# Performance work log

Measured on AMD Instinct MI355X. Metric: run time of the kernel, lower is better.

## Reference

```python
import jax, jax.numpy as jnp
import numpy as np
import math

B, H, S, D = 2, 16, 2048, 64

def setup_inputs() -> dict:
    key = jax.random.key(0)
    kq, kk, kv = jax.random.split(key, 3)
    Q = jax.random.normal(kq, (B, H, S, D), dtype=jnp.float32)
    K = jax.random.normal(kk, (B, H, S, D), dtype=jnp.float32)
    V = jax.random.normal(kv, (B, H, S, D), dtype=jnp.float32)
    # causal mask, broadcastable over batch and heads; 0 -> masked out
    mask = jnp.tril(jnp.ones((S, S), dtype=jnp.int32))[None, None, :, :]
    return {"Q": Q, "K": K, "V": V, "mask": mask}

def reference(Q, K, V, mask):
    d_k = Q.shape[-1]
    # scores: [B, H, S, S]
    scores = jnp.einsum("bhqd,bhkd->bhqk", Q, K) / math.sqrt(d_k)
    scores = jnp.where(mask == 0, jnp.float32(-1e9), scores)
    attn_weights = jax.nn.softmax(scores, axis=-1)
    output = jnp.einsum("bhqk,bhkd->bhqd", attn_weights, V)
    return (output, attn_weights)
```

## Files before the change

kernel.cpp:

```cpp
#include <hip/hip_runtime.h>
#include <hip/hip_bf16.h>


#define S_ 2048
#define D_ 64
#define BH_ 32

typedef short short8 __attribute__((ext_vector_type(8)));
typedef float f32x4 __attribute__((ext_vector_type(4)));
typedef unsigned short ushort4v __attribute__((ext_vector_type(4)));

__device__ __forceinline__ unsigned short f2bf(float f) {
  union { float f; unsigned u; } c; c.f = f;
  unsigned u = c.u + 0x7fffu + ((c.u >> 16) & 1u);
  return (unsigned short)(u >> 16);
}

__device__ __forceinline__ void g2l16(const void* g, void* l) {
  __builtin_amdgcn_global_load_lds(
      (const __attribute__((address_space(1))) unsigned int*)g,
      (__attribute__((address_space(3))) unsigned int*)l, 16, 0, 0);
}

__global__ __launch_bounds__(256) void cvt_bf16(const float* __restrict__ src,
                                                unsigned short* __restrict__ dst, int n4) {
  int i = blockIdx.x * 256 + threadIdx.x;
  if (i < n4) {
    float4 v = ((const float4*)src)[i];
    ushort4v u = { f2bf(v.x), f2bf(v.y), f2bf(v.z), f2bf(v.w) };
    ((ushort4v*)dst)[i] = u;
  }
}

__global__ __launch_bounds__(256) void vtrans(const float* __restrict__ V,
                                              unsigned short* __restrict__ Vt) {
  __shared__ float T[64][65];
  const int bh = blockIdx.x >> 5, st = blockIdx.x & 31;
  const int tid = threadIdx.x;
  const float* src = V + ((size_t)bh * S_ + st * 64) * D_;
  for (int i = tid; i < 1024; i += 256) {
    int e = i * 4; int r = e >> 6; int c = e & 63;
    float4 v = *(const float4*)(src + e);
    T[r][c] = v.x; T[r][c + 1] = v.y; T[r][c + 2] = v.z; T[r][c + 3] = v.w;
  }
  __syncthreads();
  const int d = tid >> 2;
  const int sc = (tid & 3) * 16;
  unsigned short* dst = Vt + ((size_t)bh * D_ + d) * S_ + st * 64 + sc;
#pragma unroll
  for (int j = 0; j < 16; ++j) dst[j] = f2bf(T[sc + j][d]);
}

__global__ __launch_bounds__(256, 4)
void sdpa_main(const unsigned short* __restrict__ Qg, const unsigned short* __restrict__ Kg,
               const unsigned short* __restrict__ Vtg, float* __restrict__ Og,
               float* __restrict__ Pg) {
  __shared__ __align__(16) unsigned short Kb2[2][64 * 64];
  __shared__ __align__(16) unsigned short Vb2[2][64 * 64];
  __shared__ __align__(16) unsigned short Ps[64 * 64];

  const int tid = threadIdx.x;
  const int wave = tid >> 6;
  const int lane = tid & 63;
  const int m = lane & 15;
  const int quad = lane >> 4;

  const int bh = blockIdx.x & 31;
  const int t = blockIdx.x >> 5;
  const int sg = t >> 3, g = t & 7;
  const int qb = (sg == 0) ? 16 + g : (sg == 1) ? 31 - g : (sg == 2) ? 15 - g : g;
  const int q0 = qb * 64;
  const int ktiles = qb + 1;

  const unsigned short* Kbh = Kg + (size_t)bh * S_ * D_;
  const unsigned short* Vbh = Vtg + (size_t)bh * D_ * S_;

  const unsigned short* Qrow = Qg + ((size_t)bh * S_ + q0 + wave * 16 + m) * D_;
  const short8 qf0 = *(const short8*)(Qrow + quad * 8);
  const short8 qf1 = *(const short8*)(Qrow + 32 + quad * 8);

  auto stageK = [&](const unsigned short* gbase, unsigned short* lbase) {
#pragma unroll
    for (int j = 0; j < 2; ++j) {
      int gi = wave * 2 + j;
      int row = gi * 8 + (lane >> 3);
      int c = (lane & 7) ^ (row & 7);
      g2l16(gbase + row * 64 + c * 8, lbase + gi * 512);
    }
  };
  auto stageV = [&](int kt, unsigned short* lbase) {
#pragma unroll
    for (int j = 0; j < 2; ++j) {
      int gi = wave * 2 + j;
      int d = gi * 8 + (lane >> 3);
      int c = (lane & 7) ^ (d & 7);
      g2l16(Vbh + (size_t)d * S_ + kt * 64 + c * 8, lbase + gi * 512);
    }
  };
  auto frag = [&](const unsigned short* base, int row, int kc) -> short8 {
    int c = (kc * 4 + quad) ^ (row & 7);
    return *(const short8*)(base + row * 64 + c * 8);
  };

  stageK(Kbh, Kb2[0]);
  {
    const int zc4 = (31 - qb) * 16;
    if (zc4 > 0) {
      f32x4 z = {0.f, 0.f, 0.f, 0.f};
      float* base = Pg + ((size_t)(bh * S_ + q0 + wave * 16)) * S_ + (q0 + 64);
#pragma unroll 1
      for (int r = 0; r < 16; ++r)
        for (int i = lane; i < zc4; i += 64)
          __builtin_nontemporal_store(z, (f32x4*)(base + (size_t)r * S_ + i * 4));
    }
  }

  float lsum[4] = {0.f, 0.f, 0.f, 0.f};
  for (int kt = 0; kt < ktiles; ++kt) {
    __syncthreads();
    if (kt + 1 < ktiles) stageK(Kbh + (kt + 1) * 64 * 64, Kb2[(kt + 1) & 1]);
    const unsigned short* Kt = Kb2[kt & 1];
    const bool diag = (kt == qb);
#pragma unroll
    for (int nt = 0; nt < 4; ++nt) {
      f32x4 acc = {0.f, 0.f, 0.f, 0.f};
      acc = __builtin_amdgcn_mfma_f32_16x16x32_bf16(qf0, frag(Kt, nt * 16 + m, 0), acc, 0, 0, 0);
      acc = __builtin_amdgcn_mfma_f32_16x16x32_bf16(qf1, frag(Kt, nt * 16 + m, 1), acc, 0, 0, 0);
      if (diag) {
        const int kg = kt * 64 + nt * 16 + m;
#pragma unroll
        for (int r = 0; r < 4; ++r) {
          const int qg = q0 + wave * 16 + quad * 4 + r;
          lsum[r] += (kg > qg) ? 0.f : __expf(acc[r] * 0.125f);
        }
      } else {
#pragma unroll
        for (int r = 0; r < 4; ++r) lsum[r] += __expf(acc[r] * 0.125f);
      }
    }
  }

  __syncthreads();
  stageK(Kbh, Kb2[0]);
  stageV(0, Vb2[0]);

  float invl[4];
#pragma unroll
  for (int r = 0; r < 4; ++r) {
    float v = lsum[r];
    v += __shfl_xor(v, 1); v += __shfl_xor(v, 2);
    v += __shfl_xor(v, 4); v += __shfl_xor(v, 8);
    invl[r] = 1.0f / v;
  }

  f32x4 oacc[4];
#pragma unroll
  for (int dt = 0; dt < 4; ++dt) oacc[dt] = (f32x4){0.f, 0.f, 0.f, 0.f};

  for (int kt = 0; kt < ktiles; ++kt) {
    __syncthreads();
    if (kt + 1 < ktiles) {
      stageK(Kbh + (kt + 1) * 64 * 64, Kb2[(kt + 1) & 1]);
      stageV(kt + 1, Vb2[(kt + 1) & 1]);
    }
    const unsigned short* Kt = Kb2[kt & 1];
    const unsigned short* Vt = Vb2[kt & 1];
    const bool diag = (kt == qb);
#pragma unroll
    for (int nt = 0; nt < 4; ++nt) {
      f32x4 acc = {0.f, 0.f, 0.f, 0.f};
      acc = __builtin_amdgcn_mfma_f32_16x16x32_bf16(qf0, frag(Kt, nt * 16 + m, 0), acc, 0, 0, 0);
      acc = __builtin_amdgcn_mfma_f32_16x16x32_bf16(qf1, frag(Kt, nt * 16 + m, 1), acc, 0, 0, 0);
      const int kg = kt * 64 + nt * 16 + m;
#pragma unroll
      for (int r = 0; r < 4; ++r) {
        const int qg = q0 + wave * 16 + quad * 4 + r;
        float p = (diag && kg > qg) ? 0.f : __expf(acc[r] * 0.125f) * invl[r];
        __builtin_nontemporal_store(p, Pg + (size_t)(bh * S_ + qg) * S_ + kg);
        const int prow = wave * 16 + quad * 4 + r;
        const int pcol = nt * 16 + m;
        Ps[prow * 64 + (pcol & 7) + ((((pcol >> 3) ^ (prow & 7))) << 3)] = f2bf(p);
      }
    }
#pragma unroll
    for (int dt = 0; dt < 4; ++dt)
#pragma unroll
      for (int kc = 0; kc < 2; ++kc) {
        const int prow = wave * 16 + m;
        short8 a = *(const short8*)&Ps[prow * 64 + (((kc * 4 + quad) ^ (prow & 7)) << 3)];
        short8 b = frag(Vt, dt * 16 + m, kc);
        oacc[dt] = __builtin_amdgcn_mfma_f32_16x16x32_bf16(a, b, oacc[dt], 0, 0, 0);
      }
  }

#pragma unroll
  for (int dt = 0; dt < 4; ++dt)
#pragma unroll
    for (int r = 0; r < 4; ++r)
      Og[(size_t)(bh * S_ + q0 + wave * 16 + quad * 4 + r) * D_ + dt * 16 + m] =
          oacc[dt][r];
}

extern "C" void kernel_launch(void* const* d_in, const int* in_sizes, int n_in,
                              void* d_out, int out_size, void* d_ws, size_t ws_size,
                              hipStream_t stream) {
  const float* Q = (const float*)d_in[0];
  const float* K = (const float*)d_in[1];
  const float* V = (const float*)d_in[2];
  float* Og = (float*)d_out;
  float* Pg = (float*)d_out + (size_t)BH_ * S_ * D_;

  unsigned short* Qbf = (unsigned short*)d_ws;
  unsigned short* Kbf = Qbf + (size_t)BH_ * S_ * D_;
  unsigned short* Vt  = Kbf + (size_t)BH_ * S_ * D_;

  const int n4 = (BH_ * S_ * D_) / 4;
  cvt_bf16<<<dim3(n4 / 256), dim3(256), 0, stream>>>(Q, Qbf, n4);
  cvt_bf16<<<dim3(n4 / 256), dim3(256), 0, stream>>>(K, Kbf, n4);
  vtrans<<<dim3(1024), dim3(256), 0, stream>>>(V, Vt);
  sdpa_main<<<dim3(1024), dim3(256), 0, stream>>>(Qbf, Kbf, Vt, Og, Pg);
}
```

Baseline: 666.5 us.

## Drop the separate softmax-sum pass and normalize P in a follow-up kernel

The main kernel no longer runs a first pass over all K tiles just to accumulate the exp row sums. It now writes unnormalized exp scores to P and into the LDS P tile, accumulates the row sums during the single PV pass, and scales O by the inverse sum at the end. It also stores the inverse sums so a new pnorm kernel can reread and rescale the causal part of P. Q is converted to bf16 inside the main kernel, which removes its separate conversion launch. The cost is an extra read and write of roughly half of the P matrix, traded against half of the QK MFMA and exp work.

```diff
diff --git a/kernel.cpp b/kernel.cpp
--- a/kernel.cpp
+++ b/kernel.cpp
@@ -22,11 +22,16 @@
       (__attribute__((address_space(3))) unsigned int*)l, 16, 0, 0);
 }
 
+__device__ __forceinline__ int qb_of(int t) {
+  const int sg = t >> 3, g = t & 7;
+  return (sg == 0) ? 16 + g : (sg == 1) ? 31 - g : (sg == 2) ? 15 - g : g;
+}
+
 __global__ __launch_bounds__(256) void cvt_bf16(const float* __restrict__ src,
                                                 unsigned short* __restrict__ dst, int n4) {
   int i = blockIdx.x * 256 + threadIdx.x;
   if (i < n4) {
-    float4 v = ((const float4*)src)[i];
+    f32x4 v = ((const f32x4*)src)[i];
     ushort4v u = { f2bf(v.x), f2bf(v.y), f2bf(v.z), f2bf(v.w) };
     ((ushort4v*)dst)[i] = u;
   }
@@ -40,7 +45,7 @@
   const float* src = V + ((size_t)bh * S_ + st * 64) * D_;
   for (int i = tid; i < 1024; i += 256) {
     int e = i * 4; int r = e >> 6; int c = e & 63;
-    float4 v = *(const float4*)(src + e);
+    f32x4 v = *(const f32x4*)(src + e);
     T[r][c] = v.x; T[r][c + 1] = v.y; T[r][c + 2] = v.z; T[r][c + 3] = v.w;
   }
   __syncthreads();
@@ -52,9 +57,9 @@
 }
 
 __global__ __launch_bounds__(256, 4)
-void sdpa_main(const unsigned short* __restrict__ Qg, const unsigned short* __restrict__ Kg,
+void sdpa_main(const float* __restrict__ Qg, const unsigned short* __restrict__ Kg,
                const unsigned short* __restrict__ Vtg, float* __restrict__ Og,
-               float* __restrict__ Pg) {
+               float* __restrict__ Pg, float* __restrict__ Lg) {
   __shared__ __align__(16) unsigned short Kb2[2][64 * 64];
   __shared__ __align__(16) unsigned short Vb2[2][64 * 64];
   __shared__ __align__(16) unsigned short Ps[64 * 64];
@@ -66,18 +71,25 @@
   const int quad = lane >> 4;
 
   const int bh = blockIdx.x & 31;
-  const int t = blockIdx.x >> 5;
-  const int sg = t >> 3, g = t & 7;
-  const int qb = (sg == 0) ? 16 + g : (sg == 1) ? 31 - g : (sg == 2) ? 15 - g : g;
+  const int qb = qb_of(blockIdx.x >> 5);
   const int q0 = qb * 64;
   const int ktiles = qb + 1;
 
   const unsigned short* Kbh = Kg + (size_t)bh * S_ * D_;
   const unsigned short* Vbh = Vtg + (size_t)bh * D_ * S_;
 
-  const unsigned short* Qrow = Qg + ((size_t)bh * S_ + q0 + wave * 16 + m) * D_;
-  const short8 qf0 = *(const short8*)(Qrow + quad * 8);
-  const short8 qf1 = *(const short8*)(Qrow + 32 + quad * 8);
+  const float* Qrow = Qg + ((size_t)bh * S_ + q0 + wave * 16 + m) * D_;
+  short8 qf0, qf1;
+  {
+    f32x4 a0 = *(const f32x4*)(Qrow + quad * 8);
+    f32x4 a1 = *(const f32x4*)(Qrow + quad * 8 + 4);
+    f32x4 b0 = *(const f32x4*)(Qrow + 32 + quad * 8);
+    f32x4 b1 = *(const f32x4*)(Qrow + 32 + quad * 8 + 4);
+    qf0 = (short8){(short)f2bf(a0.x), (short)f2bf(a0.y), (short)f2bf(a0.z), (short)f2bf(a0.w),
+                   (short)f2bf(a1.x), (short)f2bf(a1.y), (short)f2bf(a1.z), (short)f2bf(a1.w)};
+    qf1 = (short8){(short)f2bf(b0.x), (short)f2bf(b0.y), (short)f2bf(b0.z), (short)f2bf(b0.w),
+                   (short)f2bf(b1.x), (short)f2bf(b1.y), (short)f2bf(b1.z), (short)f2bf(b1.w)};
+  }
 
   auto stageK = [&](const unsigned short* gbase, unsigned short* lbase) {
 #pragma unroll
@@ -103,6 +115,7 @@
   };
 
   stageK(Kbh, Kb2[0]);
+  stageV(0, Vb2[0]);
   {
     const int zc4 = (31 - qb) * 16;
     if (zc4 > 0) {
@@ -116,43 +129,6 @@
   }
 
   float lsum[4] = {0.f, 0.f, 0.f, 0.f};
-  for (int kt = 0; kt < ktiles; ++kt) {
-    __syncthreads();
-    if (kt + 1 < ktiles) stageK(Kbh + (kt + 1) * 64 * 64, Kb2[(kt + 1) & 1]);
-    const unsigned short* Kt = Kb2[kt & 1];
-    const bool diag = (kt == qb);
-#pragma unroll
-    for (int nt = 0; nt < 4; ++nt) {
-      f32x4 acc = {0.f, 0.f, 0.f, 0.f};
-      acc = __builtin_amdgcn_mfma_f32_16x16x32_bf16(qf0, frag(Kt, nt * 16 + m, 0), acc, 0, 0, 0);
-      acc = __builtin_amdgcn_mfma_f32_16x16x32_bf16(qf1, frag(Kt, nt * 16 + m, 1), acc, 0, 0, 0);
-      if (diag) {
-        const int kg = kt * 64 + nt * 16 + m;
-#pragma unroll
-        for (int r = 0; r < 4; ++r) {
-          const int qg = q0 + wave * 16 + quad * 4 + r;
-          lsum[r] += (kg > qg) ? 0.f : __expf(acc[r] * 0.125f);
-        }
-      } else {
-#pragma unroll
-        for (int r = 0; r < 4; ++r) lsum[r] += __expf(acc[r] * 0.125f);
-      }
-    }
-  }
-
-  __syncthreads();
-  stageK(Kbh, Kb2[0]);
-  stageV(0, Vb2[0]);
-
-  float invl[4];
-#pragma unroll
-  for (int r = 0; r < 4; ++r) {
-    float v = lsum[r];
-    v += __shfl_xor(v, 1); v += __shfl_xor(v, 2);
-    v += __shfl_xor(v, 4); v += __shfl_xor(v, 8);
-    invl[r] = 1.0f / v;
-  }
-
   f32x4 oacc[4];
 #pragma unroll
   for (int dt = 0; dt < 4; ++dt) oacc[dt] = (f32x4){0.f, 0.f, 0.f, 0.f};
@@ -175,11 +151,12 @@
 #pragma unroll
       for (int r = 0; r < 4; ++r) {
         const int qg = q0 + wave * 16 + quad * 4 + r;
-        float p = (diag && kg > qg) ? 0.f : __expf(acc[r] * 0.125f) * invl[r];
-        __builtin_nontemporal_store(p, Pg + (size_t)(bh * S_ + qg) * S_ + kg);
+        float e = (diag && kg > qg) ? 0.f : __expf(acc[r] * 0.125f);
+        lsum[r] += e;
+        __builtin_nontemporal_store(e, Pg + (size_t)(bh * S_ + qg) * S_ + kg);
         const int prow = wave * 16 + quad * 4 + r;
         const int pcol = nt * 16 + m;
-        Ps[prow * 64 + (pcol & 7) + ((((pcol >> 3) ^ (prow & 7))) << 3)] = f2bf(p);
+        Ps[prow * 64 + (pcol & 7) + ((((pcol >> 3) ^ (prow & 7))) << 3)] = f2bf(e);
       }
     }
 #pragma unroll
@@ -193,12 +170,45 @@
       }
   }
 
+  float invl[4];
+#pragma unroll
+  for (int r = 0; r < 4; ++r) {
+    float v = lsum[r];
+    v += __shfl_xor(v, 1); v += __shfl_xor(v, 2);
+    v += __shfl_xor(v, 4); v += __shfl_xor(v, 8);
+    invl[r] = 1.0f / v;
+  }
+  if (m == 0) {
+#pragma unroll
+    for (int r = 0; r < 4; ++r)
+      Lg[bh * S_ + q0 + wave * 16 + quad * 4 + r] = invl[r];
+  }
+
 #pragma unroll
   for (int dt = 0; dt < 4; ++dt)
 #pragma unroll
     for (int r = 0; r < 4; ++r)
       Og[(size_t)(bh * S_ + q0 + wave * 16 + quad * 4 + r) * D_ + dt * 16 + m] =
-          oacc[dt][r];
+          oacc[dt][r] * invl[r];
+}
+
+__global__ __launch_bounds__(256) void pnorm(float* __restrict__ Pg,
+                                             const float* __restrict__ Lg) {
+  const int bh = blockIdx.x & 31;
+  const int qb = qb_of(blockIdx.x >> 5);
+  const int len4 = (qb + 1) * 16;
+  float* base = Pg + ((size_t)(bh * S_ + qb * 64)) * S_;
+  const float* L = Lg + bh * S_ + qb * 64;
+#pragma unroll 1
+  for (int r = 0; r < 64; ++r) {
+    const float inv = L[r];
+    f32x4* rowp = (f32x4*)(base + (size_t)r * S_);
+    for (int i = threadIdx.x; i < len4; i += 256) {
+      f32x4 v = __builtin_nontemporal_load(rowp + i);
+      v.x *= inv; v.y *= inv; v.z *= inv; v.w *= inv;
+      __builtin_nontemporal_store(v, rowp + i);
+    }
+  }
 }
 
 extern "C" void kernel_launch(void* const* d_in, const int* in_sizes, int n_in,
@@ -210,13 +220,13 @@
   float* Og = (float*)d_out;
   float* Pg = (float*)d_out + (size_t)BH_ * S_ * D_;
 
-  unsigned short* Qbf = (unsigned short*)d_ws;
-  unsigned short* Kbf = Qbf + (size_t)BH_ * S_ * D_;
+  unsigned short* Kbf = (unsigned short*)d_ws;
   unsigned short* Vt  = Kbf + (size_t)BH_ * S_ * D_;
+  float* Lg = (float*)(Vt + (size_t)BH_ * S_ * D_);
 
   const int n4 = (BH_ * S_ * D_) / 4;
-  cvt_bf16<<<dim3(n4 / 256), dim3(256), 0, stream>>>(Q, Qbf, n4);
   cvt_bf16<<<dim3(n4 / 256), dim3(256), 0, stream>>>(K, Kbf, n4);
   vtrans<<<dim3(1024), dim3(256), 0, stream>>>(V, Vt);
-  sdpa_main<<<dim3(1024), dim3(256), 0, stream>>>(Qbf, Kbf, Vt, Og, Pg);
-}
+  sdpa_main<<<dim3(1024), dim3(256), 0, stream>>>(Q, Kbf, Vt, Og, Pg, Lg);
+  pnorm<<<dim3(1024), dim3(256), 0, stream>>>(Pg, Lg);
+}
```

Result: slower. 848.7 us (+27.3%).
